# Optimization experiments

Measured on AMD Instinct MI355X. Metric: run time of the kernel, lower is better.

## Reference

```python
import jax, jax.numpy as jnp
import numpy as np

N = 100_000   # nodes
E = 1_600_000 # edges
F = 128       # num_features
D = 32        # hidden dim
G = 1000      # graphs (segments for global_add_pool)
C = 10        # num_classes
BN_EPS = 1e-5


def setup_inputs() -> dict:
    key = jax.random.key(0)
    ks = jax.random.split(key, 16)
    sc = 0.05
    x = jax.random.normal(ks[0], (N, F), jnp.float32)
    edge_index = jax.random.randint(ks[1], (2, E), 0, N)
    batch = jnp.sort(jax.random.randint(ks[2], (N,), 0, G))
    # layer-1 MLP: F -> D -> D
    W1a = jax.random.normal(ks[3], (F, D), jnp.float32) * sc
    b1a = jnp.zeros((D,), jnp.float32)
    W1b = jax.random.normal(ks[4], (D, D), jnp.float32) * sc
    b1b = jnp.zeros((D,), jnp.float32)
    # layers 2-5 MLPs stacked: D -> D -> D
    Wa = jax.random.normal(ks[5], (4, D, D), jnp.float32) * sc
    ba = jnp.zeros((4, D), jnp.float32)
    Wb = jax.random.normal(ks[6], (4, D, D), jnp.float32) * sc
    bb = jnp.zeros((4, D), jnp.float32)
    # BatchNorm affine params for 5 BN layers
    gamma = jnp.ones((5, D), jnp.float32)
    beta = jnp.zeros((5, D), jnp.float32)
    fc1_w = jax.random.normal(ks[7], (D, D), jnp.float32) * sc
    fc1_b = jnp.zeros((D,), jnp.float32)
    fc2_w = jax.random.normal(ks[8], (D, C), jnp.float32) * sc
    fc2_b = jnp.zeros((C,), jnp.float32)
    return dict(x=x, edge_index=edge_index, batch=batch,
                W1a=W1a, b1a=b1a, W1b=W1b, b1b=b1b,
                Wa=Wa, ba=ba, Wb=Wb, bb=bb,
                gamma=gamma, beta=beta,
                fc1_w=fc1_w, fc1_b=fc1_b, fc2_w=fc2_w, fc2_b=fc2_b)


def _gin_conv(h, src, dst, wa, ba_, wb, bb_):
    # GINConv (eps=0): nn(x + sum_{j->i} x_j); messages flow src=row0 -> dst=row1
    agg = jax.ops.segment_sum(h[src], dst, num_segments=N)
    h = h + agg
    h = jnp.maximum(h @ wa + ba_, 0.0) @ wb + bb_
    return h


def _bn(h, g, b):
    # BatchNorm1d, training-mode batch stats (biased variance)
    m = h.mean(axis=0)
    v = h.var(axis=0)
    return g * (h - m) * jax.lax.rsqrt(v + BN_EPS) + b


def reference(x, edge_index, batch, W1a, b1a, W1b, b1b, Wa, ba, Wb, bb,
              gamma, beta, fc1_w, fc1_b, fc2_w, fc2_b):
    src, dst = edge_index[0], edge_index[1]
    h = jnp.maximum(_gin_conv(x, src, dst, W1a, b1a, W1b, b1b), 0.0)
    h = _bn(h, gamma[0], beta[0])
    for i in range(4):  # fixed small layer count
        h = jnp.maximum(_gin_conv(h, src, dst, Wa[i], ba[i], Wb[i], bb[i]), 0.0)
        h = _bn(h, gamma[i + 1], beta[i + 1])
    # global_add_pool over graphs
    pooled = jax.ops.segment_sum(h, batch, num_segments=G)  # [G, D]
    h = jnp.maximum(pooled @ fc1_w + fc1_b, 0.0)
    # dropout is identity in eval mode
    logits = h @ fc2_w + fc2_b
    return jax.nn.log_softmax(logits, axis=-1)
```

## Files before the change

### kernel.cpp

```cpp
#include <hip/hip_runtime.h>
#include <hip/hip_bf16.h>
#include <hip/hip_fp16.h>

#define NN 100000
#define EE 1600000
#define FF 128
#define DD 32
#define GG 1000
#define CC 10
#define BN_EPS 1e-5f
#define REC 48
#define CAPE 47
#define NB64 1563

__device__ __forceinline__ void up8(uint4 u, float* f) {
    __half2* h = (__half2*)&u;
#pragma unroll
    for (int i = 0; i < 4; i++) {
        float2 t = __half22float2(h[i]);
        f[2 * i] = t.x; f[2 * i + 1] = t.y;
    }
}

__device__ __forceinline__ void acc8(float* acc, uint4 u) {
    __half2* h = (__half2*)&u;
#pragma unroll
    for (int i = 0; i < 4; i++) {
        float2 t = __half22float2(h[i]);
        acc[2 * i] += t.x; acc[2 * i + 1] += t.y;
    }
}

__device__ __forceinline__ void gather_accum(float* acc, const uint4* __restrict__ V4,
                                             const int* __restrict__ sp, int deg, int sub) {
    int e = 0;
    for (; e + 8 <= deg; e += 8) {
        int4 sa = *(const int4*)(sp + e);
        int4 sb = *(const int4*)(sp + e + 4);
        uint4 u0 = V4[(long)sa.x * 4 + sub];
        uint4 u1 = V4[(long)sa.y * 4 + sub];
        uint4 u2 = V4[(long)sa.z * 4 + sub];
        uint4 u3 = V4[(long)sa.w * 4 + sub];
        uint4 u4 = V4[(long)sb.x * 4 + sub];
        uint4 u5 = V4[(long)sb.y * 4 + sub];
        uint4 u6 = V4[(long)sb.z * 4 + sub];
        uint4 u7 = V4[(long)sb.w * 4 + sub];
        acc8(acc, u0); acc8(acc, u1); acc8(acc, u2); acc8(acc, u3);
        acc8(acc, u4); acc8(acc, u5); acc8(acc, u6); acc8(acc, u7);
    }
    for (; e + 4 <= deg; e += 4) {
        int4 ss = *(const int4*)(sp + e);
        uint4 u0 = V4[(long)ss.x * 4 + sub];
        uint4 u1 = V4[(long)ss.y * 4 + sub];
        uint4 u2 = V4[(long)ss.z * 4 + sub];
        uint4 u3 = V4[(long)ss.w * 4 + sub];
        acc8(acc, u0); acc8(acc, u1); acc8(acc, u2); acc8(acc, u3);
    }
    for (; e < deg; e++) acc8(acc, V4[(long)sp[e] * 4 + sub]);
}

__global__ __launch_bounds__(256) void k_prep(const int* __restrict__ src,
                                              const int* __restrict__ dst,
                                              int* __restrict__ rec,
                                              const float* __restrict__ x,
                                              const float* __restrict__ W,
                                              __half* __restrict__ t) {
    __shared__ float Wl[FF * DD];
    __shared__ float xs[16 * FF];
    int bid = blockIdx.x;
    int tid = threadIdx.x;
    if (bid & 1) {
        int gid = bid >> 1;
        const float4* W4 = (const float4*)W;
        float4* Wl4 = (float4*)Wl;
        for (int i = tid; i < FF * DD / 4; i += 256) Wl4[i] = W4[i];
        long node0 = (long)gid * 16;
        const float4* x4 = (const float4*)(x + node0 * FF);
        float4* xs4 = (float4*)xs;
        for (int i = tid; i < 16 * FF / 4; i += 256) xs4[i] = x4[i];
        __syncthreads();
        int tx = tid & 31, ty = tid >> 5;
        float a0 = 0.f, a1 = 0.f;
#pragma unroll 8
        for (int k = 0; k < FF; k++) {
            float w = Wl[k * DD + tx];
            a0 += xs[ty * FF + k] * w;
            a1 += xs[(ty + 8) * FF + k] * w;
        }
        t[(node0 + ty) * DD + tx] = __float2half_rn(a0);
        t[(node0 + ty + 8) * DD + tx] = __float2half_rn(a1);
    } else {
        int e = (bid >> 1) * 256 + tid;
        int d = dst[e];
        int p = atomicAdd(&rec[d * REC + CAPE], 1);
        if (p < CAPE) rec[d * REC + p] = src[e];
    }
}

__global__ __launch_bounds__(256) void k_fused1(const uint4* __restrict__ T4,
                                                const int* __restrict__ rec,
                                                const float* __restrict__ b1a,
                                                const float* __restrict__ W1b,
                                                const float* __restrict__ b1b,
                                                __half* __restrict__ vout,
                                                float* __restrict__ S) {
    __shared__ float U[64 * DD];
    __shared__ float ssum[DD], ssq[DD];
    int tid = threadIdx.x;
    if (tid < DD) { ssum[tid] = 0.f; ssq[tid] = 0.f; }
    int g4 = tid >> 2, sub = tid & 3;
    int n = blockIdx.x * 64 + g4;
    if (n < NN) {
        float acc[8];
        up8(T4[(long)n * 4 + sub], acc);
        const int* sp = rec + n * REC;
        int deg = sp[CAPE]; if (deg > CAPE) deg = CAPE;
        gather_accum(acc, T4, sp, deg, sub);
#pragma unroll
        for (int j = 0; j < 8; j++)
            U[g4 * DD + sub * 8 + j] = fmaxf(acc[j] + b1a[sub * 8 + j], 0.f);
    } else {
#pragma unroll
        for (int j = 0; j < 8; j++) U[g4 * DD + sub * 8 + j] = 0.f;
    }
    __syncthreads();
    int tx = tid & 31, ty = tid >> 5;
    float w[DD];
#pragma unroll
    for (int k = 0; k < DD; k++) w[k] = W1b[k * DD + tx];
    float bb = b1b[tx];
    float sl = 0.f, sq = 0.f;
#pragma unroll
    for (int m = 0; m < 8; m++) {
        int node = ty + 8 * m;
        int nn = blockIdx.x * 64 + node;
        float a = bb;
        const float4* h4 = (const float4*)(U + node * DD);
#pragma unroll
        for (int k4 = 0; k4 < 8; k4++) {
            float4 h = h4[k4];
            a += h.x * w[4 * k4] + h.y * w[4 * k4 + 1] + h.z * w[4 * k4 + 2] + h.w * w[4 * k4 + 3];
        }
        if (nn < NN) {
            float hv = fmaxf(a, 0.f);
            vout[(long)nn * DD + tx] = __float2half_rn(hv);
            sl += hv; sq += hv * hv;
        }
    }
    atomicAdd(&ssum[tx], sl);
    atomicAdd(&ssq[tx], sq);
    __syncthreads();
    if (tid < DD) {
        unsafeAtomicAdd(&S[tid], ssum[tid]);
        unsafeAtomicAdd(&S[DD + tid], ssq[tid]);
    }
}

__global__ __launch_bounds__(256) void k_fusedN(const uint4* __restrict__ Vin4,
                                                const int* __restrict__ rec,
                                                const float* __restrict__ Sprev,
                                                const float* __restrict__ gamma,
                                                const float* __restrict__ beta,
                                                const float* __restrict__ wa,
                                                const float* __restrict__ ba,
                                                const float* __restrict__ wb,
                                                const float* __restrict__ bb,
                                                __half* __restrict__ vout,
                                                float* __restrict__ S) {
    __shared__ float Hs[64 * DD];
    __shared__ float U[64 * DD];
    __shared__ float ssum[DD], ssq[DD], scl[DD], shl[DD];
    int tid = threadIdx.x;
    if (tid < DD) {
        ssum[tid] = 0.f; ssq[tid] = 0.f;
        float mean = Sprev[tid] * (1.0f / NN);
        float var = Sprev[DD + tid] * (1.0f / NN) - mean * mean;
        float inv = rsqrtf(var + BN_EPS);
        float sc = gamma[tid] * inv;
        scl[tid] = sc;
        shl[tid] = beta[tid] - mean * sc;
    }
    __syncthreads();
    int g4 = tid >> 2, sub = tid & 3;
    int n = blockIdx.x * 64 + g4;
    if (n < NN) {
        float acc[8];
        up8(Vin4[(long)n * 4 + sub], acc);
        const int* sp = rec + n * REC;
        int deg = sp[CAPE]; if (deg > CAPE) deg = CAPE;
        gather_accum(acc, Vin4, sp, deg, sub);
        float d1 = (float)(1 + deg);
#pragma unroll
        for (int j = 0; j < 8; j++) {
            int f = sub * 8 + j;
            Hs[g4 * DD + f] = scl[f] * acc[j] + d1 * shl[f];
        }
    } else {
#pragma unroll
        for (int j = 0; j < 8; j++) Hs[g4 * DD + sub * 8 + j] = 0.f;
    }
    __syncthreads();
    int tx = tid & 31, ty = tid >> 5;
    {
        float w[DD];
#pragma unroll
        for (int k = 0; k < DD; k++) w[k] = wa[k * DD + tx];
        float bal = ba[tx];
#pragma unroll
        for (int m = 0; m < 8; m++) {
            int node = ty + 8 * m;
            float a = bal;
            const float4* h4 = (const float4*)(Hs + node * DD);
#pragma unroll
            for (int k4 = 0; k4 < 8; k4++) {
                float4 h = h4[k4];
                a += h.x * w[4 * k4] + h.y * w[4 * k4 + 1] + h.z * w[4 * k4 + 2] + h.w * w[4 * k4 + 3];
            }
            U[node * DD + tx] = fmaxf(a, 0.f);
        }
    }
    __syncthreads();
    {
        float w[DD];
#pragma unroll
        for (int k = 0; k < DD; k++) w[k] = wb[k * DD + tx];
        float bbl = bb[tx];
        float sl = 0.f, sq = 0.f;
#pragma unroll
        for (int m = 0; m < 8; m++) {
            int node = ty + 8 * m;
            int nn = blockIdx.x * 64 + node;
            float a = bbl;
            const float4* h4 = (const float4*)(U + node * DD);
#pragma unroll
            for (int k4 = 0; k4 < 8; k4++) {
                float4 h = h4[k4];
                a += h.x * w[4 * k4] + h.y * w[4 * k4 + 1] + h.z * w[4 * k4 + 2] + h.w * w[4 * k4 + 3];
            }
            if (nn < NN) {
                float hv = fmaxf(a, 0.f);
                vout[(long)nn * DD + tx] = __float2half_rn(hv);
                sl += hv; sq += hv * hv;
            }
        }
        atomicAdd(&ssum[tx], sl);
        atomicAdd(&ssq[tx], sq);
    }
    __syncthreads();
    if (tid < DD) {
        unsafeAtomicAdd(&S[tid], ssum[tid]);
        unsafeAtomicAdd(&S[DD + tid], ssq[tid]);
    }
}

__global__ __launch_bounds__(256) void k_pool(const __half* __restrict__ v,
                                              const float* __restrict__ Sprev,
                                              const float* __restrict__ gamma,
                                              const float* __restrict__ beta,
                                              const int* __restrict__ batch,
                                              float* __restrict__ pooled) {
    __shared__ float scl[DD], shl[DD];
    int tid = threadIdx.x;
    if (tid < DD) {
        float mean = Sprev[tid] * (1.0f / NN);
        float var = Sprev[DD + tid] * (1.0f / NN) - mean * mean;
        float inv = rsqrtf(var + BN_EPS);
        float sc = gamma[tid] * inv;
        scl[tid] = sc;
        shl[tid] = beta[tid] - mean * sc;
    }
    __syncthreads();
    int tx = tid & 31, ty = tid >> 5;
    float sc = scl[tx], sh = shl[tx];
    int n0 = blockIdx.x * 256 + ty * 32;
    int cur = -1; float run = 0.f;
    for (int i = 0; i < 32; i++) {
        int n = n0 + i;
        if (n >= NN) break;
        int b = batch[n];
        float val = __half2float(v[(long)n * DD + tx]) * sc + sh;
        if (b != cur) {
            if (cur >= 0) unsafeAtomicAdd(&pooled[(long)cur * DD + tx], run);
            run = 0.f; cur = b;
        }
        run += val;
    }
    if (cur >= 0) unsafeAtomicAdd(&pooled[(long)cur * DD + tx], run);
}

__global__ __launch_bounds__(256) void k_head(const float* __restrict__ pooled,
                                              const float* __restrict__ fc1w,
                                              const float* __restrict__ fc1b,
                                              const float* __restrict__ fc2w,
                                              const float* __restrict__ fc2b,
                                              float* __restrict__ out) {
    __shared__ float W1[DD * DD], B1[DD], W2[DD * CC], B2[CC];
    int tid = threadIdx.x;
    for (int i = tid; i < DD * DD; i += 256) W1[i] = fc1w[i];
    for (int i = tid; i < DD * CC; i += 256) W2[i] = fc2w[i];
    if (tid < DD) B1[tid] = fc1b[tid];
    if (tid < CC) B2[tid] = fc2b[tid];
    __syncthreads();
    int g = blockIdx.x * 256 + tid;
    if (g >= GG) return;
    float p[DD];
#pragma unroll
    for (int d = 0; d < DD; d++) p[d] = pooled[(long)g * DD + d];
    float h[DD];
#pragma unroll
    for (int d = 0; d < DD; d++) {
        float acc = B1[d];
#pragma unroll
        for (int k = 0; k < DD; k++) acc += p[k] * W1[k * DD + d];
        h[d] = fmaxf(acc, 0.f);
    }
    float lg[CC];
#pragma unroll
    for (int c = 0; c < CC; c++) {
        float acc = B2[c];
#pragma unroll
        for (int d = 0; d < DD; d++) acc += h[d] * W2[d * CC + c];
        lg[c] = acc;
    }
    float m = lg[0];
#pragma unroll
    for (int c = 1; c < CC; c++) m = fmaxf(m, lg[c]);
    float s = 0.f;
#pragma unroll
    for (int c = 0; c < CC; c++) s += __expf(lg[c] - m);
    float ls = logf(s);
#pragma unroll
    for (int c = 0; c < CC; c++) out[(long)g * CC + c] = lg[c] - m - ls;
}

extern "C" void kernel_launch(void* const* d_in, const int* in_sizes, int n_in,
                              void* d_out, int out_size, void* d_ws, size_t ws_size,
                              hipStream_t stream) {
    const float* x    = (const float*)d_in[0];
    const int* ei     = (const int*)d_in[1];
    const int* batch  = (const int*)d_in[2];
    const float* W1a  = (const float*)d_in[3];
    const float* b1a  = (const float*)d_in[4];
    const float* W1b  = (const float*)d_in[5];
    const float* b1b  = (const float*)d_in[6];
    const float* Wa   = (const float*)d_in[7];
    const float* ba   = (const float*)d_in[8];
    const float* Wb   = (const float*)d_in[9];
    const float* bb   = (const float*)d_in[10];
    const float* gm   = (const float*)d_in[11];
    const float* bt   = (const float*)d_in[12];
    const float* fc1w = (const float*)d_in[13];
    const float* fc1b = (const float*)d_in[14];
    const float* fc2w = (const float*)d_in[15];
    const float* fc2b = (const float*)d_in[16];

    char* base = (char*)d_ws;
    __half* Th   = (__half*)base;
    __half* Vh   = (__half*)(base + 6400000);
    float*  S    = (float*)(base + 12800000);
    float*  POOL = (float*)(base + 12801536);
    int*    rec  = (int*)(base + 12929536);

    const int* esrc = ei;
    const int* edst = ei + EE;

    hipMemsetAsync(base + 12800000, 0, (size_t)19335680, stream);

    k_prep<<<12500, 256, 0, stream>>>(esrc, edst, rec, x, W1a, Th);

    k_fused1<<<NB64, 256, 0, stream>>>((const uint4*)Th, rec,
                                       b1a, W1b, b1b, Vh, S);

    __half* bufs[2] = {Vh, Th};
    for (int j = 0; j < 4; j++) {
        k_fusedN<<<NB64, 256, 0, stream>>>((const uint4*)bufs[j & 1], rec,
                                           S + j * 64, gm + j * 32, bt + j * 32,
                                           Wa + j * 1024, ba + j * 32,
                                           Wb + j * 1024, bb + j * 32,
                                           bufs[(j + 1) & 1], S + (j + 1) * 64);
    }

    k_pool<<<(NN + 255) / 256, 256, 0, stream>>>(Vh, S + 4 * 64, gm + 4 * 32,
                                                 bt + 4 * 32, batch, POOL);
    k_head<<<(GG + 255) / 256, 256, 0, stream>>>(POOL, fc1w, fc1b, fc2w, fc2b,
                                                 (float*)d_out);
}
```

Baseline: 546.5 us.

## Build the adjacency with a two-pass bucketed binning instead of global atomics

Edge-to-destination adjacency construction is now done in two passes. The first bins edges by destination block into per-bucket packed arrays, using shared-memory staging and one global atomic per bucket per chunk. The second pass builds each bucket's per-node record list with shared-memory atomics and writes the counts directly, so the large memset of the record array is no longer needed. The x@W1a projection now handles 32 nodes per block. Fixed capacities (64 per chunk-bucket, 17280 per bucket) risk silently dropping edges if the input distribution is skewed.

```diff
diff --git a/kernel.cpp b/kernel.cpp
--- a/kernel.cpp
+++ b/kernel.cpp
@@ -12,6 +12,13 @@
 #define REC 48
 #define CAPE 47
 #define NB64 1563
+
+#define NBUCK 98
+#define BSH 10
+#define BCAP 17280
+#define CCAP 64
+#define CHUNK 2048
+#define NCHUNK 782
 
 __device__ __forceinline__ void up8(uint4 u, float* f) {
     __half2* h = (__half2*)&u;
@@ -59,41 +66,96 @@
     for (; e < deg; e++) acc8(acc, V4[(long)sp[e] * 4 + sub]);
 }
 
-__global__ __launch_bounds__(256) void k_prep(const int* __restrict__ src,
-                                              const int* __restrict__ dst,
-                                              int* __restrict__ rec,
-                                              const float* __restrict__ x,
-                                              const float* __restrict__ W,
-                                              __half* __restrict__ t) {
-    __shared__ float Wl[FF * DD];
-    __shared__ float xs[16 * FF];
-    int bid = blockIdx.x;
+__global__ __launch_bounds__(256) void k_bin(const int* __restrict__ src,
+                                             const int* __restrict__ dst,
+                                             int* __restrict__ gcur,
+                                             int* __restrict__ pack) {
+    __shared__ int bcnt[NBUCK];
+    __shared__ int bbase[NBUCK];
+    __shared__ int bbuf[NBUCK * CCAP];
     int tid = threadIdx.x;
-    if (bid & 1) {
-        int gid = bid >> 1;
+    for (int i = tid; i < NBUCK; i += 256) bcnt[i] = 0;
+    __syncthreads();
+    int e0 = blockIdx.x * CHUNK;
+#pragma unroll
+    for (int i = 0; i < CHUNK / 256; i++) {
+        int e = e0 + i * 256 + tid;
+        if (e < EE) {
+            int d = dst[e], s = src[e];
+            int b = d >> BSH;
+            int p = atomicAdd(&bcnt[b], 1);
+            if (p < CCAP) bbuf[b * CCAP + p] = ((d & ((1 << BSH) - 1)) << 17) | s;
+        }
+    }
+    __syncthreads();
+    for (int b = tid; b < NBUCK; b += 256) {
+        int c = bcnt[b]; if (c > CCAP) c = CCAP;
+        bbase[b] = atomicAdd(&gcur[b], c);
+    }
+    __syncthreads();
+    for (int b = 0; b < NBUCK; b++) {
+        int c = bcnt[b]; if (c > CCAP) c = CCAP;
+        int gb = bbase[b];
+        for (int i = tid; i < c; i += 256) {
+            int idx = gb + i;
+            if (idx >= 0 && idx < BCAP) pack[b * BCAP + idx] = bbuf[b * CCAP + i];
+        }
+    }
+}
+
+__global__ __launch_bounds__(256) void k_prep2(const int* __restrict__ gcur,
+                                               const int* __restrict__ pack,
+                                               int* __restrict__ rec,
+                                               const float* __restrict__ x,
+                                               const float* __restrict__ W,
+                                               __half* __restrict__ t) {
+    __shared__ float sh[FF * DD + 32 * FF];
+    int bid = blockIdx.x, tid = threadIdx.x;
+    if (bid < NBUCK) {
+        int* lcnt = (int*)sh;
+        for (int i = tid; i < (1 << BSH); i += 256) lcnt[i] = 0;
+        __syncthreads();
+        int m = gcur[bid]; if (m > BCAP) m = BCAP;
+        const int* pk = pack + bid * BCAP;
+        int nb = bid << BSH;
+        for (int i = tid; i < m; i += 256) {
+            int w = pk[i];
+            int s = w & 0x1FFFF;
+            int dl = w >> 17;
+            int p = atomicAdd(&lcnt[dl], 1);
+            if (p < CAPE) rec[(nb + dl) * REC + p] = s;
+        }
+        __syncthreads();
+        for (int dl = tid; dl < (1 << BSH); dl += 256) {
+            int d = nb + dl;
+            if (d < NN) rec[d * REC + CAPE] = lcnt[dl];
+        }
+    } else {
+        float* Wl = sh;
+        float* xs = sh + FF * DD;
+        int gid = bid - NBUCK;
         const float4* W4 = (const float4*)W;
         float4* Wl4 = (float4*)Wl;
         for (int i = tid; i < FF * DD / 4; i += 256) Wl4[i] = W4[i];
-        long node0 = (long)gid * 16;
+        long node0 = (long)gid * 32;
         const float4* x4 = (const float4*)(x + node0 * FF);
         float4* xs4 = (float4*)xs;
-        for (int i = tid; i < 16 * FF / 4; i += 256) xs4[i] = x4[i];
+        for (int i = tid; i < 32 * FF / 4; i += 256) xs4[i] = x4[i];
         __syncthreads();
         int tx = tid & 31, ty = tid >> 5;
-        float a0 = 0.f, a1 = 0.f;
+        float a0 = 0.f, a1 = 0.f, a2 = 0.f, a3 = 0.f;
 #pragma unroll 8
         for (int k = 0; k < FF; k++) {
             float w = Wl[k * DD + tx];
             a0 += xs[ty * FF + k] * w;
             a1 += xs[(ty + 8) * FF + k] * w;
+            a2 += xs[(ty + 16) * FF + k] * w;
+            a3 += xs[(ty + 24) * FF + k] * w;
         }
         t[(node0 + ty) * DD + tx] = __float2half_rn(a0);
         t[(node0 + ty + 8) * DD + tx] = __float2half_rn(a1);
-    } else {
-        int e = (bid >> 1) * 256 + tid;
-        int d = dst[e];
-        int p = atomicAdd(&rec[d * REC + CAPE], 1);
-        if (p < CAPE) rec[d * REC + p] = src[e];
+        t[(node0 + ty + 16) * DD + tx] = __float2half_rn(a2);
+        t[(node0 + ty + 24) * DD + tx] = __float2half_rn(a3);
     }
 }
 
@@ -357,16 +419,22 @@
     char* base = (char*)d_ws;
     __half* Th   = (__half*)base;
     __half* Vh   = (__half*)(base + 6400000);
-    float*  S    = (float*)(base + 12800000);
-    float*  POOL = (float*)(base + 12801536);
-    int*    rec  = (int*)(base + 12929536);
+    int*    pack = (int*)(base + 6400000);
+    float*  S    = (float*)(base + 13173760);
+    float*  POOL = (float*)(base + 13175040);
+    int*    gcur = (int*)(base + 13303040);
+    int*    rec  = (int*)(base + 13303552);
 
     const int* esrc = ei;
     const int* edst = ei + EE;
 
-    hipMemsetAsync(base + 12800000, 0, (size_t)19335680, stream);
-
-    k_prep<<<12500, 256, 0, stream>>>(esrc, edst, rec, x, W1a, Th);
+    hipMemsetAsync(gcur, 0, 512, stream);
+
+    k_bin<<<NCHUNK, 256, 0, stream>>>(esrc, edst, gcur, pack);
+
+    k_prep2<<<NBUCK + 3125, 256, 0, stream>>>(gcur, pack, rec, x, W1a, Th);
+
+    hipMemsetAsync(S, 0, 129280, stream);
 
     k_fused1<<<NB64, 256, 0, stream>>>((const uint4*)Th, rec,
                                        b1a, W1b, b1b, Vh, S);
```

Result: faster. 524.3 us (-4.1%).
